# Kernel tuning notes

Measured on AMD Instinct MI355X. Metric: run time of the kernel, lower is better.

The kernel has to match this reference:

```python
import jax, jax.numpy as jnp
import numpy as np
import math

B, S, HID = 2, 4096, 768
H, D, M = 12, 64, 64  # heads, head_dim, num_landmarks
CK = 33  # conv kernel size


def setup_inputs() -> dict:
    key = jax.random.key(0)
    ks = jax.random.split(key, 4)
    x = jax.random.normal(ks[0], (B, S, HID), dtype=jnp.float32)
    qkv_w = jax.random.normal(ks[1], (3 * HID, HID), dtype=jnp.float32) * 0.02
    qkv_b = jnp.zeros((3 * HID,), dtype=jnp.float32)
    conv_w = jax.random.normal(ks[2], (H, 1, CK, 1), dtype=jnp.float32) * 0.02
    out_w = jax.random.normal(ks[3], (HID, HID), dtype=jnp.float32) * 0.02
    out_b = jnp.zeros((HID,), dtype=jnp.float32)
    return {"x": x, "qkv_w": qkv_w, "qkv_b": qkv_b, "conv_w": conv_w,
            "out_w": out_w, "out_b": out_b}


def iterative_inv(mat, n_iter=6):
    # Newton-Schulz pseudo-inverse on [B,H,M,M]
    I = jnp.eye(mat.shape[-1], dtype=mat.dtype)
    K = mat
    a = jnp.abs(K)
    scale = 1.0 / (jnp.max(jnp.sum(a, axis=-2)) * jnp.max(jnp.sum(a, axis=-1)))
    V = scale * jnp.swapaxes(K, -1, -2)
    for _ in range(n_iter):
        KV = K @ V
        V = 0.25 * V @ (13.0 * I - KV @ (15.0 * I - KV @ (7.0 * I - KV)))
    return V


def reference(x, qkv_w, qkv_b, conv_w, out_w, out_b):
    scale = 1.0 / math.sqrt(D)
    qkv = x @ qkv_w.T + qkv_b  # [B,S,3*HID]
    q, k, v = jnp.split(qkv, 3, axis=-1)
    # [B,H,S,D]
    Q = q.reshape(B, S, H, D).transpose(0, 2, 1, 3)
    K = k.reshape(B, S, H, D).transpose(0, 2, 1, 3)
    V = v.reshape(B, S, H, D).transpose(0, 2, 1, 3)
    # landmark means over contiguous segments of size S//M
    seg = S // M
    Q_l = Q.reshape(B, H, M, seg, D).mean(axis=-2)  # [B,H,M,D]
    K_l = K.reshape(B, H, M, seg, D).mean(axis=-2)
    kernel_1 = jax.nn.softmax(jnp.einsum('bhsd,bhmd->bhsm', Q, K_l) * scale, axis=-1)
    kernel_2 = jax.nn.softmax(jnp.einsum('bhmd,bhnd->bhmn', Q_l, K_l) * scale, axis=-1)
    kernel_3 = jax.nn.softmax(jnp.einsum('bhmd,bhsd->bhms', Q_l, K) * scale, axis=-1)
    X = kernel_1 @ (iterative_inv(kernel_2) @ (kernel_3 @ V))  # [B,H,S,D]
    # depthwise conv over sequence dim: NCHW with C=H, spatial=(S,D), kernel (CK,1)
    pad = CK // 2
    conv_out = jax.lax.conv_general_dilated(
        V, conv_w, window_strides=(1, 1), padding=((pad, pad), (0, 0)),
        dimension_numbers=('NCHW', 'OIHW', 'NCHW'), feature_group_count=H)
    X = X + conv_out
    X = X.transpose(0, 2, 1, 3).reshape(B, S, HID)
    X = X @ out_w.T + out_b
    return X
```

## Files before the change

kernel.cpp:

```cpp
#include <hip/hip_runtime.h>
#include <math.h>

#define B_   2
#define S_   4096
#define HID_ 768
#define H_   12
#define D_   64
#define M_   64
#define CK_  33
#define BH_  (B_*H_)
#define KD_  768
#define NCH_ 32
#define SC_  128

typedef float  f32x4  __attribute__((ext_vector_type(4)));
typedef _Float16 f16x8 __attribute__((ext_vector_type(8)));
typedef unsigned short u16;

__device__ __forceinline__ u16 f2h_bits(float f) {
  union { _Float16 h; u16 u; } c; c.h = (_Float16)f; return c.u;
}
__device__ __forceinline__ float h2f(u16 b) {
  union { _Float16 h; u16 u; } c; c.u = b; return (float)c.h;
}
__device__ __forceinline__ void cvt8_hl(const float4 a, const float4 b,
                                        f16x8* hi, f16x8* lo) {
  const float v[8] = {a.x, a.y, a.z, a.w, b.x, b.y, b.z, b.w};
  f16x8 H, L;
#pragma unroll
  for (int e = 0; e < 8; ++e) {
    const _Float16 hh = (_Float16)v[e];
    H[e] = hh;
    L[e] = (_Float16)(v[e] - (float)hh);
  }
  *hi = H; *lo = L;
}
__device__ __forceinline__ void wsplit(u16* Hh, u16* Hl, int idx, float v) {
  const _Float16 hh = (_Float16)v;
  Hh[idx] = f2h_bits(v);
  Hl[idx] = f2h_bits(v - (float)hh);
}

__device__ __forceinline__ void gld16(const void* g, void* l) {
  __builtin_amdgcn_global_load_lds(
      (const __attribute__((address_space(1))) void*)g,
      (__attribute__((address_space(3))) void*)l, 16, 0, 0);
}

#define N8X  786432
#define N8WQ 221184
#define N8WO 73728
__global__ __launch_bounds__(256) void split3(
    const float* __restrict__ x, const float* __restrict__ qkv_w,
    const float* __restrict__ out_w,
    u16* __restrict__ Xh, u16* __restrict__ Wqh, u16* __restrict__ Woh)
{
  const int i = blockIdx.x * 256 + threadIdx.x;
  const float* src; u16* dst; int j;
  if (i < N8X)                 { src = x;     dst = Xh;  j = i; }
  else if (i < N8X + N8WQ)     { src = qkv_w; dst = Wqh; j = i - N8X; }
  else if (i < N8X + N8WQ + N8WO) { src = out_w; dst = Woh; j = i - N8X - N8WQ; }
  else return;
  const float4 a = ((const float4*)src)[2 * j], b = ((const float4*)src)[2 * j + 1];
  const float v[8] = {a.x, a.y, a.z, a.w, b.x, b.y, b.z, b.w};
  union { u16 u[8]; uint4 q; } hv;
#pragma unroll
  for (int e = 0; e < 8; ++e) hv.u[e] = f2h_bits(v[e]);
  ((uint4*)dst)[j] = hv.q;
}

template<int MODE, int PROD>
__global__ __launch_bounds__(256) void gemm_mfma(
    const u16* __restrict__ Ahg, const u16* __restrict__ Alg,
    const u16* __restrict__ Bhg,
    const float* __restrict__ bias,
    float* __restrict__ oF, u16* __restrict__ oQ, u16* __restrict__ oK,
    u16* __restrict__ oV,
    float* __restrict__ Ql, float* __restrict__ Kl, u16* __restrict__ Klh)
{
  constexpr int BM = (MODE == 0) ? 128 : 64;
  constexpr int BN = (MODE == 0) ? 64 : 128;
  constexpr int NBX = (MODE == 0) ? 36 : 6;
  constexpr int WM = BM / 2, WN = BN / 2;
  constexpr int MF = WM / 16, NF = WN / 16;
  constexpr int AINST = BM / 64, BINST = BN / 64;
  constexpr int ABUF = BM * 32;
  constexpr int BUFSZ = ABUF * PROD + BN * 32;
  constexpr int NT = KD_ / 32;
  constexpr int NWG = NBX * (8192 / BM);
  constexpr int CPX = NWG / 8;
  constexpr int NLOADS = AINST * PROD + BINST;

  __shared__ __align__(16) u16 lds[2][BUFSZ];

  const int tid = threadIdx.x;
  const int lin = blockIdx.y * NBX + blockIdx.x;
  const int swb = (lin & 7) * CPX + (lin >> 3);
  const int m0 = (swb / NBX) * BM;
  const int n0 = (swb % NBX) * BN;

  const int wave = tid >> 6, lane = tid & 63;
  const int wm = wave >> 1, wn = wave & 1;
  const int lr = lane & 15, kg = lane >> 4;

  const int srow = tid >> 2;
  const int swz_s = (tid >> 3) & 3;
  const int sk = ((tid & 3) ^ swz_s) * 8;

  const u16* pAh = Ahg + (size_t)(m0 + srow) * KD_ + sk;
  const u16* pAl = (PROD == 2) ? (Alg + (size_t)(m0 + srow) * KD_ + sk) : nullptr;
  const u16* pBh = Bhg + (size_t)(n0 + srow) * KD_ + sk;

  f32x4 acc[MF][NF];
#pragma unroll
  for (int i = 0; i < MF; ++i)
#pragma unroll
    for (int j = 0; j < NF; ++j) acc[i][j] = (f32x4){0.f, 0.f, 0.f, 0.f};

  const int rsw = (lr >> 1) & 3;
  const int kq = (kg ^ rsw) * 8;
  const int abase = (wm * WM + lr) * 32 + kq;
  const int bbase = (wn * WN + lr) * 32 + kq;

#define STAGE_(buf, kt) do {                                              \
    const size_t go_ = (size_t)(kt) * 32;                                 \
    u16* L_ = &lds[buf][0];                                               \
    gld16(pAh + go_, L_ + tid * 8);                                       \
    if (AINST == 2) gld16(pAh + go_ + 64 * KD_, L_ + 2048 + tid * 8);     \
    if (PROD == 2) {                                                      \
      gld16(pAl + go_, L_ + ABUF + tid * 8);                              \
      if (AINST == 2) gld16(pAl + go_ + 64 * KD_, L_ + ABUF + 2048 + tid * 8); \
    }                                                                     \
    gld16(pBh + go_, L_ + ABUF * PROD + tid * 8);                         \
    if (BINST == 2) gld16(pBh + go_ + 64 * KD_, L_ + ABUF * PROD + 2048 + tid * 8); \
  } while (0)

  STAGE_(0, 0);

  int cur = 0;
  for (int kt = 0; kt < NT; ++kt) {
    if (kt + 1 < NT) {
      STAGE_(cur ^ 1, kt + 1);
      if constexpr (NLOADS == 3)
        asm volatile("s_waitcnt vmcnt(3)" ::: "memory");
      else
        asm volatile("s_waitcnt vmcnt(4)" ::: "memory");
    } else {
      asm volatile("s_waitcnt vmcnt(0)" ::: "memory");
    }
    __builtin_amdgcn_s_barrier();
    __builtin_amdgcn_sched_barrier(0);

    const u16* L_ = &lds[cur][0];
    f16x8 ah[MF], al[MF], bh[NF];
#pragma unroll
    for (int i = 0; i < MF; ++i) {
      ah[i] = *(const f16x8*)&L_[abase + i * 512];
      if (PROD == 2) al[i] = *(const f16x8*)&L_[ABUF + abase + i * 512];
    }
#pragma unroll
    for (int j = 0; j < NF; ++j)
      bh[j] = *(const f16x8*)&L_[ABUF * PROD + bbase + j * 512];
#pragma unroll
    for (int i = 0; i < MF; ++i)
#pragma unroll
      for (int j = 0; j < NF; ++j) {
        acc[i][j] = __builtin_amdgcn_mfma_f32_16x16x32_f16(ah[i], bh[j], acc[i][j], 0, 0, 0);
        if (PROD == 2)
          acc[i][j] = __builtin_amdgcn_mfma_f32_16x16x32_f16(al[i], bh[j], acc[i][j], 0, 0, 0);
      }

    __builtin_amdgcn_sched_barrier(0);
    __builtin_amdgcn_s_barrier();
    cur ^= 1;
  }
#undef STAGE_

  if (MODE == 0) {
    const int part = n0 / 768;
    const int h0 = (n0 - part * 768) >> 6;
    u16* base = (part == 0) ? oQ : ((part == 1) ? oK : oV);
#pragma unroll
    for (int i = 0; i < MF; ++i) {
      const int mbase = m0 + wm * WM + i * 16 + kg * 4;
#pragma unroll
      for (int j = 0; j < NF; ++j) {
        const int d = wn * WN + j * 16 + lr;
        const float bv = bias[n0 + d];
#pragma unroll
        for (int r = 0; r < 4; ++r) {
          const int row = mbase + r;
          const int b = row >> 12, s = row & (S_ - 1);
          base[(((size_t)(b * H_ + h0) * S_ + s) << 6) + d] = f2h_bits(acc[i][j][r] + bv);
        }
      }
    }
    if (part < 2) {
      const int rowseg = m0 + wm * WM;
      const int b = rowseg >> 12;
      const int seg = (rowseg & (S_ - 1)) >> 6;
      const int bhh = b * H_ + h0;
      float* dst = (part == 0) ? Ql : Kl;
#pragma unroll
      for (int j = 0; j < NF; ++j) {
        float sj = 0.f;
#pragma unroll
        for (int i = 0; i < MF; ++i)
#pragma unroll
          for (int r = 0; r < 4; ++r) sj += acc[i][j][r];
        sj += __shfl_xor(sj, 16);
        sj += __shfl_xor(sj, 32);
        if (kg == 0) {
          const int d = wn * WN + j * 16 + lr;
          const float lm = sj * (1.f / 64.f) + bias[n0 + d];
          dst[((size_t)bhh * M_ + seg) * 64 + d] = lm;
          if (part == 1) Klh[((size_t)bhh * M_ + seg) * 64 + d] = f2h_bits(lm);
        }
      }
    }
  } else {
#pragma unroll
    for (int i = 0; i < MF; ++i) {
      const int mbase = m0 + wm * WM + i * 16 + kg * 4;
#pragma unroll
      for (int j = 0; j < NF; ++j) {
        const int ncol = n0 + wn * WN + j * 16 + lr;
        const float bv = bias[ncol];
#pragma unroll
        for (int r = 0; r < 4; ++r) {
          const int row = mbase + r;
          oF[(size_t)row * HID_ + ncol] = acc[i][j][r] + bv;
        }
      }
    }
  }
}

__global__ __launch_bounds__(256) void kernel2_softmax(
    const float* __restrict__ Ql, const float* __restrict__ Kl,
    float* __restrict__ K2, float* __restrict__ colmax, float* __restrict__ rowmax)
{
  __shared__ float Qs[64][68], Ks[64][68], S2[64][68];
  __shared__ float red1[64], red2[64];
  const int bh = blockIdx.x, tid = threadIdx.x;
  for (int idx = tid; idx < 4096; idx += 256) {
    const int r = idx >> 6, c = idx & 63;
    Qs[r][c] = Ql[(size_t)bh * 4096 + idx];
    Ks[r][c] = Kl[(size_t)bh * 4096 + idx];
  }
  __syncthreads();
  for (int idx = tid; idx < 4096; idx += 256) {
    const int r = idx >> 6, c = idx & 63;
    float dot = 0.f;
#pragma unroll
    for (int k = 0; k < 64; k += 4) {
      const float4 a = *(const float4*)&Qs[r][k];
      const float4 b = *(const float4*)&Ks[c][k];
      dot += a.x * b.x + a.y * b.y + a.z * b.z + a.w * b.w;
    }
    S2[r][c] = dot * 0.125f;
  }
  __syncthreads();
  if (tid < 64) {
    const int r = tid;
    float mx = -1e30f;
    for (int c = 0; c < 64; ++c) mx = fmaxf(mx, S2[r][c]);
    float sum = 0.f;
    for (int c = 0; c < 64; ++c) { const float e = expf(S2[r][c] - mx); S2[r][c] = e; sum += e; }
    const float inv = 1.f / sum;
    for (int c = 0; c < 64; ++c) S2[r][c] *= inv;
  }
  __syncthreads();
  for (int idx = tid; idx < 4096; idx += 256)
    K2[(size_t)bh * 4096 + idx] = S2[idx >> 6][idx & 63];
  if (tid < 64) {
    float cs = 0.f, rs = 0.f;
    for (int m = 0; m < 64; ++m) { cs += S2[m][tid]; rs += S2[tid][m]; }
    red1[tid] = cs; red2[tid] = rs;
  }
  __syncthreads();
  if (tid == 0) {
    float mc = 0.f, mr = 0.f;
    for (int i = 0; i < 64; ++i) { mc = fmaxf(mc, red1[i]); mr = fmaxf(mr, red2[i]); }
    colmax[bh] = mc; rowmax[bh] = mr;
  }
}

#define NST 88
__device__ __forceinline__ void mfma64x64(
    const u16* Ah, const u16* Al, const u16* Bh, const u16* Bl,
    int wave, int lr, int kg, f32x4 C[4])
{
#pragma unroll
  for (int j = 0; j < 4; ++j) C[j] = (f32x4){0.f, 0.f, 0.f, 0.f};
#pragma unroll
  for (int kk = 0; kk < 2; ++kk) {
    const int ao = (wave * 16 + lr) * NST + kk * 32 + kg * 8;
    const f16x8 ah = *(const f16x8*)&Ah[ao];
    const f16x8 al = *(const f16x8*)&Al[ao];
#pragma unroll
    for (int j = 0; j < 4; ++j) {
      const int bo = (j * 16 + lr) * NST + kk * 32 + kg * 8;
      const f16x8 bh = *(const f16x8*)&Bh[bo];
      const f16x8 bl = *(const f16x8*)&Bl[bo];
      C[j] = __builtin_amdgcn_mfma_f32_16x16x32_f16(ah, bh, C[j], 0, 0, 0);
      C[j] = __builtin_amdgcn_mfma_f32_16x16x32_f16(ah, bl, C[j], 0, 0, 0);
      C[j] = __builtin_amdgcn_mfma_f32_16x16x32_f16(al, bh, C[j], 0, 0, 0);
    }
  }
}

__global__ __launch_bounds__(256) void newton_combine(
    const float* __restrict__ K2, const float* __restrict__ colmax,
    const float* __restrict__ rowmax,
    const float* __restrict__ Opart, const float* __restrict__ mpart,
    const float* __restrict__ lpart, float* __restrict__ W2)
{
  __shared__ __align__(16) u16 K2h[64*NST], K2l[64*NST];
  __shared__ __align__(16) u16 Vh_[64*NST], Vl_[64*NST];
  __shared__ __align__(16) u16 VTh[64*NST], VTl[64*NST];
  __shared__ __align__(16) u16 KVh[64*NST], KVl[64*NST];
  __shared__ __align__(16) u16 TTh[64*NST], TTl[64*NST];
  __shared__ float w_[64][33];
  __shared__ float scale_s;

  const int bh = blockIdx.x, tid = threadIdx.x;
  const int wave = tid >> 6, lane = tid & 63;
  const int lr = lane & 15, kg = lane >> 4;

  if (tid == 0) {
    float mc = 0.f, mr = 0.f;
    for (int i = 0; i < BH_; ++i) { mc = fmaxf(mc, colmax[i]); mr = fmaxf(mr, rowmax[i]); }
    scale_s = 1.f / (mc * mr);
  }
  __syncthreads();
  const float scale = scale_s;

  for (int idx = tid; idx < 4096; idx += 256) {
    const int r = idx >> 6, c = idx & 63;
    const float v = K2[(size_t)bh * 4096 + idx];
    wsplit(K2h, K2l, r * NST + c, v);
    const float sv = scale * v;
    wsplit(VTh, VTl, r * NST + c, sv);
    wsplit(Vh_, Vl_, c * NST + r, sv);
  }
  __syncthreads();

  f32x4 C[4];
  for (int it = 0; it < 6; ++it) {
    mfma64x64(K2h, K2l, VTh, VTl, wave, lr, kg, C);
#pragma unroll
    for (int j = 0; j < 4; ++j)
#pragma unroll
      for (int r = 0; r < 4; ++r) {
        const int row = wave * 16 + kg * 4 + r, col = j * 16 + lr;
        const float kv = C[j][r];
        wsplit(KVh, KVl, row * NST + col, kv);
        wsplit(TTh, TTl, col * NST + row, (row == col ? 7.f : 0.f) - kv);
      }
    __syncthreads();
    mfma64x64(KVh, KVl, TTh, TTl, wave, lr, kg, C);
    __syncthreads();
#pragma unroll
    for (int j = 0; j < 4; ++j)
#pragma unroll
      for (int r = 0; r < 4; ++r) {
        const int row = wave * 16 + kg * 4 + r, col = j * 16 + lr;
        wsplit(TTh, TTl, col * NST + row, (row == col ? 15.f : 0.f) - C[j][r]);
      }
    __syncthreads();
    mfma64x64(KVh, KVl, TTh, TTl, wave, lr, kg, C);
    __syncthreads();
#pragma unroll
    for (int j = 0; j < 4; ++j)
#pragma unroll
      for (int r = 0; r < 4; ++r) {
        const int row = wave * 16 + kg * 4 + r, col = j * 16 + lr;
        wsplit(TTh, TTl, col * NST + row, (row == col ? 13.f : 0.f) - C[j][r]);
      }
    __syncthreads();
    mfma64x64(Vh_, Vl_, TTh, TTl, wave, lr, kg, C);
#pragma unroll
    for (int j = 0; j < 4; ++j)
#pragma unroll
      for (int r = 0; r < 4; ++r) {
        const int row = wave * 16 + kg * 4 + r, col = j * 16 + lr;
        const float v = 0.25f * C[j][r];
        wsplit(Vh_, Vl_, row * NST + col, v);
        wsplit(VTh, VTl, col * NST + row, v);
      }
    __syncthreads();
  }

  if (tid < 64) {
    const int m = tid;
    float Mx = -1e30f;
    for (int j = 0; j < NCH_; ++j)
      Mx = fmaxf(Mx, mpart[((size_t)bh * NCH_ + j) * 64 + m]);
    float denom = 0.f;
    for (int j = 0; j < NCH_; ++j)
      denom += expf(mpart[((size_t)bh * NCH_ + j) * 64 + m] - Mx) *
               lpart[((size_t)bh * NCH_ + j) * 64 + m];
    const float inv = 1.f / denom;
    for (int j = 0; j < NCH_; ++j)
      w_[m][j] = expf(mpart[((size_t)bh * NCH_ + j) * 64 + m] - Mx) * inv;
  }
  __syncthreads();
  u16* W1Th = K2h;
  u16* W1Tl = K2l;
  {
    const int mg = tid >> 4, dq = (tid & 15) * 4;
#pragma unroll
    for (int i = 0; i < 4; ++i) {
      const int m = mg * 4 + i;
      float4 acc = make_float4(0.f, 0.f, 0.f, 0.f);
      for (int j = 0; j < NCH_; ++j) {
        const float ww = w_[m][j];
        const float4 o = *(const float4*)&Opart[(((size_t)bh * NCH_ + j) * 64 + m) * 64 + dq];
        acc.x += ww * o.x; acc.y += ww * o.y; acc.z += ww * o.z; acc.w += ww * o.w;
      }
      wsplit(W1Th, W1Tl, (dq + 0) * NST + m, acc.x);
      wsplit(W1Th, W1Tl, (dq + 1) * NST + m, acc.y);
      wsplit(W1Th, W1Tl, (dq + 2) * NST + m, acc.z);
      wsplit(W1Th, W1Tl, (dq + 3) * NST + m, acc.w);
    }
  }
  __syncthreads();
  mfma64x64(Vh_, Vl_, W1Th, W1Tl, wave, lr, kg, C);
#pragma unroll
  for (int j = 0; j < 4; ++j)
#pragma unroll
    for (int r = 0; r < 4; ++r) {
      const int row = wave * 16 + kg * 4 + r, col = j * 16 + lr;
      W2[(size_t)bh * 4096 + row * 64 + col] = C[j][r];
    }
}

__global__ __launch_bounds__(256) void k3v_pass1(
    const float* __restrict__ Ql, const u16* __restrict__ Kh,
    const u16* __restrict__ Vh, float* __restrict__ Opart,
    float* __restrict__ mpart, float* __restrict__ lpart)
{
  __shared__ float P[64][129];
  __shared__ float red1[64][4], red2[64][4];

  const int ch = blockIdx.x;
  const int bh = blockIdx.y;
  const int tid = threadIdx.x;
  const int wave = tid >> 6, lane = tid & 63;
  const int lr = lane & 15, kg = lane >> 4;

  const float* Qlb = Ql + (size_t)bh * 4096;
  const u16*   Kb  = Kh + (size_t)bh * S_ * 64;
  const u16*   Vb  = Vh + (size_t)bh * S_ * 64;

  f16x8 ah[4][2], al[4][2];
#pragma unroll
  for (int mt = 0; mt < 4; ++mt)
#pragma unroll
    for (int kk = 0; kk < 2; ++kk) {
      const float* qr = Qlb + (size_t)(mt * 16 + lr) * 64 + kk * 32 + kg * 8;
      cvt8_hl(*(const float4*)qr, *(const float4*)(qr + 4), &ah[mt][kk], &al[mt][kk]);
    }

#pragma unroll
  for (int t = 0; t < 2; ++t) {
    const int s0 = (wave * 2 + t) * 16;
    const int srow = ch * SC_ + s0 + lr;
    f32x4 acc[4];
#pragma unroll
    for (int mt = 0; mt < 4; ++mt) acc[mt] = (f32x4){0.f, 0.f, 0.f, 0.f};
#pragma unroll
    for (int kk = 0; kk < 2; ++kk) {
      const f16x8 bhf = *(const f16x8*)&Kb[(size_t)srow * 64 + kk * 32 + kg * 8];
#pragma unroll
      for (int mt = 0; mt < 4; ++mt) {
        acc[mt] = __builtin_amdgcn_mfma_f32_16x16x32_f16(ah[mt][kk], bhf, acc[mt], 0, 0, 0);
        acc[mt] = __builtin_amdgcn_mfma_f32_16x16x32_f16(al[mt][kk], bhf, acc[mt], 0, 0, 0);
      }
    }
#pragma unroll
    for (int mt = 0; mt < 4; ++mt)
#pragma unroll
      for (int r = 0; r < 4; ++r)
        P[mt * 16 + kg * 4 + r][s0 + lr] = acc[mt][r] * 0.125f;
  }
  __syncthreads();

  const int r = tid >> 2, q = tid & 3;
  {
    float mx = -1e30f;
#pragma unroll
    for (int s = 0; s < 32; ++s) mx = fmaxf(mx, P[r][q * 32 + s]);
    red1[r][q] = mx;
  }
  __syncthreads();
  const float rowmax = fmaxf(fmaxf(red1[r][0], red1[r][1]),
                             fmaxf(red1[r][2], red1[r][3]));
  {
    float sum = 0.f;
#pragma unroll
    for (int s = 0; s < 32; ++s) {
      const float e = expf(P[r][q * 32 + s] - rowmax);
      P[r][q * 32 + s] = e;
      sum += e;
    }
    red2[r][q] = sum;
  }
  __syncthreads();
  if (q == 0) {
    const float rowsum = red2[r][0] + red2[r][1] + red2[r][2] + red2[r][3];
    mpart[((size_t)bh * NCH_ + ch) * 64 + r] = rowmax;
    lpart[((size_t)bh * NCH_ + ch) * 64 + r] = rowsum;
  }

  const int mg = tid >> 4, dq = (tid & 15) * 4;
  float4 oacc[4];
#pragma unroll
  for (int i = 0; i < 4; ++i) oacc[i] = make_float4(0.f, 0.f, 0.f, 0.f);
  for (int s = 0; s < SC_; ++s) {
    const ushort4 vv = *(const ushort4*)&Vb[(size_t)(ch * SC_ + s) * 64 + dq];
    const float4 v = make_float4(h2f(vv.x), h2f(vv.y), h2f(vv.z), h2f(vv.w));
#pragma unroll
    for (int i = 0; i < 4; ++i) {
      const float p = P[mg * 4 + i][s];
      oacc[i].x += p * v.x; oacc[i].y += p * v.y;
      oacc[i].z += p * v.z; oacc[i].w += p * v.w;
    }
  }
#pragma unroll
  for (int i = 0; i < 4; ++i) {
    const size_t o = (((size_t)bh * NCH_ + ch) * 64 + mg * 4 + i) * 64 + dq;
    *(float4*)&Opart[o] = oacc[i];
  }
}

__global__ __launch_bounds__(256) void attn_conv_fused(
    const u16* __restrict__ Qh, const u16* __restrict__ Klh,
    const float* __restrict__ W2, const u16* __restrict__ Vh,
    const float* __restrict__ cw,
    u16* __restrict__ Xch, u16* __restrict__ Xcl)
{
  __shared__ __align__(16) u16 smem[19456];
  __shared__ float cws[33];

  const int ch = blockIdx.x;
  const int bh = blockIdx.y;
  const int tid = threadIdx.x;
  const int wave = tid >> 6, lane = tid & 63;
  const int lr = lane & 15, kg = lane >> 4;
  const int b = bh / H_, h = bh % H_;
  const int s0 = ch * 128;

  u16* Ph   = smem;
  u16* W2Th = smem + 9728;
  u16* W2Tl = smem + 14592;

  if (tid < 33) cws[tid] = cw[h * 33 + tid];
  for (int idx = tid; idx < 4096; idx += 256) {
    const int m = idx >> 6, d = idx & 63;
    const float w = W2[(size_t)bh * 4096 + idx];
    const _Float16 hh = (_Float16)w;
    W2Th[d * 76 + m] = f2h_bits(w);
    W2Tl[d * 76 + m] = f2h_bits(w - (float)hh);
  }

  const u16* Klb = Klh + (size_t)bh * 4096;
  const u16* Qb  = Qh + (size_t)bh * S_ * 64;
  f16x8 bf[4][2];
#pragma unroll
  for (int nt = 0; nt < 4; ++nt)
#pragma unroll
    for (int kk = 0; kk < 2; ++kk)
      bf[nt][kk] = *(const f16x8*)&Klb[(size_t)(nt * 16 + lr) * 64 + kk * 32 + kg * 8];

  f32x4 sacc[2][4];
#pragma unroll
  for (int t = 0; t < 2; ++t) {
#pragma unroll
    for (int nt = 0; nt < 4; ++nt) sacc[t][nt] = (f32x4){0.f, 0.f, 0.f, 0.f};
    const int rloc = wave * 32 + t * 16;
    f16x8 af[2];
#pragma unroll
    for (int kk = 0; kk < 2; ++kk)
      af[kk] = *(const f16x8*)&Qb[(size_t)(s0 + rloc + lr) * 64 + kk * 32 + kg * 8];
#pragma unroll
    for (int kk = 0; kk < 2; ++kk)
#pragma unroll
      for (int nt = 0; nt < 4; ++nt)
        sacc[t][nt] = __builtin_amdgcn_mfma_f32_16x16x32_f16(af[kk], bf[nt][kk], sacc[t][nt], 0, 0, 0);
  }

#pragma unroll
  for (int t = 0; t < 2; ++t)
#pragma unroll
    for (int nt = 0; nt < 4; ++nt)
      sacc[t][nt] *= 0.125f;

  float rinv[2][4];
#pragma unroll
  for (int t = 0; t < 2; ++t) {
#pragma unroll
    for (int r = 0; r < 4; ++r) {
      float mx = fmaxf(fmaxf(sacc[t][0][r], sacc[t][1][r]),
                       fmaxf(sacc[t][2][r], sacc[t][3][r]));
      mx = fmaxf(mx, __shfl_xor(mx, 1));
      mx = fmaxf(mx, __shfl_xor(mx, 2));
      mx = fmaxf(mx, __shfl_xor(mx, 4));
      mx = fmaxf(mx, __shfl_xor(mx, 8));
      float sum = 0.f;
#pragma unroll
      for (int nt = 0; nt < 4; ++nt) {
        const float e = expf(sacc[t][nt][r] - mx);
        sacc[t][nt][r] = e;
        sum += e;
      }
      sum += __shfl_xor(sum, 1);
      sum += __shfl_xor(sum, 2);
      sum += __shfl_xor(sum, 4);
      sum += __shfl_xor(sum, 8);
      rinv[t][r] = 1.f / sum;
    }
  }

#pragma unroll
  for (int t = 0; t < 2; ++t)
#pragma unroll
    for (int nt = 0; nt < 4; ++nt)
#pragma unroll
      for (int r = 0; r < 4; ++r) {
        const int row = wave * 32 + t * 16 + kg * 4 + r;
        Ph[row * 76 + nt * 16 + lr] = f2h_bits(sacc[t][nt][r] * rinv[t][r]);
      }
  __syncthreads();

  f32x4 oacc[2][4];
#pragma unroll
  for (int t = 0; t < 2; ++t)
#pragma unroll
    for (int dt = 0; dt < 4; ++dt) oacc[t][dt] = (f32x4){0.f, 0.f, 0.f, 0.f};
#pragma unroll
  for (int kk = 0; kk < 2; ++kk) {
    f16x8 pa[2];
#pragma unroll
    for (int t = 0; t < 2; ++t)
      pa[t] = *(const f16x8*)&Ph[(wave * 32 + t * 16 + lr) * 76 + kk * 32 + kg * 8];
#pragma unroll
    for (int dt = 0; dt < 4; ++dt) {
      const f16x8 wh = *(const f16x8*)&W2Th[(dt * 16 + lr) * 76 + kk * 32 + kg * 8];
      const f16x8 wl = *(const f16x8*)&W2Tl[(dt * 16 + lr) * 76 + kk * 32 + kg * 8];
#pragma unroll
      for (int t = 0; t < 2; ++t) {
        oacc[t][dt] = __builtin_amdgcn_mfma_f32_16x16x32_f16(pa[t], wh, oacc[t][dt], 0, 0, 0);
        oacc[t][dt] = __builtin_amdgcn_mfma_f32_16x16x32_f16(pa[t], wl, oacc[t][dt], 0, 0, 0);
      }
    }
  }
  __syncthreads();

  float* O = (float*)smem;
#pragma unroll
  for (int t = 0; t < 2; ++t)
#pragma unroll
    for (int dt = 0; dt < 4; ++dt)
#pragma unroll
      for (int r = 0; r < 4; ++r) {
        const int row = wave * 32 + t * 16 + kg * 4 + r;
        O[row * 68 + dt * 16 + lr] = oacc[t][dt][r];
      }
  __syncthreads();

  const int d = tid & 63, rg = tid >> 6;
  const int rbase = s0 + rg * 32;
  const u16* Vd = Vh + (size_t)bh * S_ * 64 + d;

  float v[40];
#pragma unroll
  for (int j = 0; j < 40; ++j) {
    const int sv = rbase - 16 + j;
    v[j] = (sv >= 0 && sv < S_) ? h2f(Vd[(size_t)sv * 64]) : 0.f;
  }

#pragma clang loop unroll(disable)
  for (int c = 0; c < 4; ++c) {
#pragma unroll
    for (int rr = 0; rr < 8; ++rr) {
      float acc = 0.f;
#pragma unroll
      for (int t = 0; t < 33; ++t) acc += v[rr + t] * cws[t];
      const int row = rg * 32 + c * 8 + rr;
      const float oo = O[row * 68 + d] + acc;
      const size_t idx = ((size_t)(b * S_ + s0 + row)) * HID_ + h * 64 + d;
      const u16 hh = f2h_bits(oo);
      Xch[idx] = hh;
      Xcl[idx] = f2h_bits(oo - h2f(hh));
    }
    if (c < 3) {
#pragma unroll
      for (int j = 0; j < 32; ++j) v[j] = v[j + 8];
#pragma unroll
      for (int j = 0; j < 8; ++j) {
        const int sv = rbase + 24 + c * 8 + j;
        v[32 + j] = (sv >= 0 && sv < S_) ? h2f(Vd[(size_t)sv * 64]) : 0.f;
      }
    }
  }
}

extern "C" void kernel_launch(void* const* d_in, const int* in_sizes, int n_in,
                              void* d_out, int out_size, void* d_ws, size_t ws_size,
                              hipStream_t stream)
{
  (void)in_sizes; (void)n_in; (void)out_size; (void)ws_size;
  const float* x      = (const float*)d_in[0];
  const float* qkv_w  = (const float*)d_in[1];
  const float* qkv_b  = (const float*)d_in[2];
  const float* conv_w = (const float*)d_in[3];
  const float* out_w  = (const float*)d_in[4];
  const float* out_b  = (const float*)d_in[5];
  float* out = (float*)d_out;

  float* ws = (float*)d_ws;
  u16* Qh = (u16*)ws;
  u16* Kh = Qh + 6291456;
  u16* Vh = Kh + 6291456;
  float* Ql = ws + 9437184;
  float* Kl = Ql + 98304;
  float* K2 = Kl + 98304;
  float* W2 = K2 + 98304;
  float* colmax = W2 + 98304;
  float* rowmax = colmax + 32;
  u16* Klh = (u16*)(rowmax + 32);
  float* nxt = rowmax + 32 + 49152;
  u16* Xh  = (u16*)nxt;
  u16* Xl  = Xh + 6291456;
  u16* Wqh = Xl + 6291456;
  u16* Woh = Wqh + 1769472;
  u16* Xch = Xh;
  u16* Xcl = Xl;
  float* Opart = (float*)Xh;
  float* mpart = (float*)Xl;
  float* lpart = mpart + BH_ * NCH_ * 64;

  split3<<<(N8X + N8WQ + N8WO + 255) / 256, 256, 0, stream>>>(
      x, qkv_w, out_w, Xh, Wqh, Woh);

  gemm_mfma<0, 1><<<dim3(36, 64), 256, 0, stream>>>(
      Xh, nullptr, Wqh, qkv_b, nullptr, Qh, Kh, Vh, Ql, Kl, Klh);

  kernel2_softmax<<<BH_, 256, 0, stream>>>(Ql, Kl, K2, colmax, rowmax);

  k3v_pass1<<<dim3(NCH_, BH_), 256, 0, stream>>>(Ql, Kh, Vh, Opart, mpart, lpart);

  newton_combine<<<BH_, 256, 0, stream>>>(K2, colmax, rowmax,
                                          Opart, mpart, lpart, W2);

  attn_conv_fused<<<dim3(NCH_, BH_), 256, 0, stream>>>(
      Qh, Klh, W2, Vh, conv_w, Xch, Xcl);

  gemm_mfma<1, 2><<<dim3(6, 128), 256, 0, stream>>>(
      Xch, Xcl, Woh, out_b, out, nullptr, nullptr, nullptr,
      nullptr, nullptr, nullptr);
}
```

Before: 212.3 us.

## Use per-wave private LDS tiles in GEMMs and drop fp16 split-precision output

```diff
diff --git a/kernel.cpp b/kernel.cpp
--- a/kernel.cpp
+++ b/kernel.cpp
@@ -69,124 +69,102 @@
   ((uint4*)dst)[j] = hv.q;
 }
 
-template<int MODE, int PROD>
-__global__ __launch_bounds__(256) void gemm_mfma(
-    const u16* __restrict__ Ahg, const u16* __restrict__ Alg,
-    const u16* __restrict__ Bhg,
+template<int MODE>
+__global__ __launch_bounds__(256) void gemm_wave(
+    const u16* __restrict__ Ahg, const u16* __restrict__ Bhg,
     const float* __restrict__ bias,
     float* __restrict__ oF, u16* __restrict__ oQ, u16* __restrict__ oK,
     u16* __restrict__ oV,
     float* __restrict__ Ql, float* __restrict__ Kl, u16* __restrict__ Klh)
 {
-  constexpr int BM = (MODE == 0) ? 128 : 64;
-  constexpr int BN = (MODE == 0) ? 64 : 128;
-  constexpr int NBX = (MODE == 0) ? 36 : 6;
-  constexpr int WM = BM / 2, WN = BN / 2;
-  constexpr int MF = WM / 16, NF = WN / 16;
-  constexpr int AINST = BM / 64, BINST = BN / 64;
-  constexpr int ABUF = BM * 32;
-  constexpr int BUFSZ = ABUF * PROD + BN * 32;
-  constexpr int NT = KD_ / 32;
-  constexpr int NWG = NBX * (8192 / BM);
+  constexpr int NBX = (MODE == 0) ? 18 : 6;
+  constexpr int NT  = KD_ / 32;
+  constexpr int NWG = NBX * 64;
   constexpr int CPX = NWG / 8;
-  constexpr int NLOADS = AINST * PROD + BINST;
-
-  __shared__ __align__(16) u16 lds[2][BUFSZ];
+
+  __shared__ __align__(16) u16 lds[4][2][2][2048];
 
   const int tid = threadIdx.x;
   const int lin = blockIdx.y * NBX + blockIdx.x;
   const int swb = (lin & 7) * CPX + (lin >> 3);
-  const int m0 = (swb / NBX) * BM;
-  const int n0 = (swb % NBX) * BN;
+  const int m0 = (swb / NBX) * 128;
+  const int n0 = (swb % NBX) * 128;
 
   const int wave = tid >> 6, lane = tid & 63;
   const int wm = wave >> 1, wn = wave & 1;
   const int lr = lane & 15, kg = lane >> 4;
 
-  const int srow = tid >> 2;
-  const int swz_s = (tid >> 3) & 3;
-  const int sk = ((tid & 3) ^ swz_s) * 8;
-
-  const u16* pAh = Ahg + (size_t)(m0 + srow) * KD_ + sk;
-  const u16* pAl = (PROD == 2) ? (Alg + (size_t)(m0 + srow) * KD_ + sk) : nullptr;
-  const u16* pBh = Bhg + (size_t)(n0 + srow) * KD_ + sk;
-
-  f32x4 acc[MF][NF];
-#pragma unroll
-  for (int i = 0; i < MF; ++i)
-#pragma unroll
-    for (int j = 0; j < NF; ++j) acc[i][j] = (f32x4){0.f, 0.f, 0.f, 0.f};
-
-  const int rsw = (lr >> 1) & 3;
-  const int kq = (kg ^ rsw) * 8;
-  const int abase = (wm * WM + lr) * 32 + kq;
-  const int bbase = (wn * WN + lr) * 32 + kq;
-
-#define STAGE_(buf, kt) do {                                              \
-    const size_t go_ = (size_t)(kt) * 32;                                 \
-    u16* L_ = &lds[buf][0];                                               \
-    gld16(pAh + go_, L_ + tid * 8);                                       \
-    if (AINST == 2) gld16(pAh + go_ + 64 * KD_, L_ + 2048 + tid * 8);     \
-    if (PROD == 2) {                                                      \
-      gld16(pAl + go_, L_ + ABUF + tid * 8);                              \
-      if (AINST == 2) gld16(pAl + go_ + 64 * KD_, L_ + ABUF + 2048 + tid * 8); \
-    }                                                                     \
-    gld16(pBh + go_, L_ + ABUF * PROD + tid * 8);                         \
-    if (BINST == 2) gld16(pBh + go_ + 64 * KD_, L_ + ABUF * PROD + 2048 + tid * 8); \
+  const int srow = lane >> 2;
+  const int sk = ((lane & 3) ^ ((lane >> 3) & 3)) * 8;
+
+  const u16* pA = Ahg + (size_t)(m0 + wm * 64 + srow) * KD_ + sk;
+  const u16* pB = Bhg + (size_t)(n0 + wn * 64 + srow) * KD_ + sk;
+
+  u16* wbase = &lds[wave][0][0][0];
+
+  f32x4 acc[4][4];
+#pragma unroll
+  for (int i = 0; i < 4; ++i)
+#pragma unroll
+    for (int j = 0; j < 4; ++j) acc[i][j] = (f32x4){0.f, 0.f, 0.f, 0.f};
+
+  const int kq = (kg ^ ((lr >> 1) & 3)) * 8;
+
+#define WSTAGE_(buf, kt) do {                                   \
+    const size_t go_ = (size_t)(kt) * 32;                       \
+    u16* La_ = wbase + (buf) * 4096 + lane * 8;                 \
+    u16* Lb_ = La_ + 2048;                                      \
+    gld16(pA + go_,              La_);                          \
+    gld16(pA + go_ + 16 * KD_,   La_ + 512);                    \
+    gld16(pA + go_ + 32 * KD_,   La_ + 1024);                   \
+    gld16(pA + go_ + 48 * KD_,   La_ + 1536);                   \
+    gld16(pB + go_,              Lb_);                          \
+    gld16(pB + go_ + 16 * KD_,   Lb_ + 512);                    \
+    gld16(pB + go_ + 32 * KD_,   Lb_ + 1024);                   \
+    gld16(pB + go_ + 48 * KD_,   Lb_ + 1536);                   \
   } while (0)
 
-  STAGE_(0, 0);
+  WSTAGE_(0, 0);
 
   int cur = 0;
   for (int kt = 0; kt < NT; ++kt) {
     if (kt + 1 < NT) {
-      STAGE_(cur ^ 1, kt + 1);
-      if constexpr (NLOADS == 3)
-        asm volatile("s_waitcnt vmcnt(3)" ::: "memory");
-      else
-        asm volatile("s_waitcnt vmcnt(4)" ::: "memory");
+      WSTAGE_(cur ^ 1, kt + 1);
+      asm volatile("s_waitcnt vmcnt(8)" ::: "memory");
     } else {
       asm volatile("s_waitcnt vmcnt(0)" ::: "memory");
     }
-    __builtin_amdgcn_s_barrier();
     __builtin_amdgcn_sched_barrier(0);
 
-    const u16* L_ = &lds[cur][0];
-    f16x8 ah[MF], al[MF], bh[NF];
-#pragma unroll
-    for (int i = 0; i < MF; ++i) {
-      ah[i] = *(const f16x8*)&L_[abase + i * 512];
-      if (PROD == 2) al[i] = *(const f16x8*)&L_[ABUF + abase + i * 512];
-    }
-#pragma unroll
-    for (int j = 0; j < NF; ++j)
-      bh[j] = *(const f16x8*)&L_[ABUF * PROD + bbase + j * 512];
-#pragma unroll
-    for (int i = 0; i < MF; ++i)
-#pragma unroll
-      for (int j = 0; j < NF; ++j) {
-        acc[i][j] = __builtin_amdgcn_mfma_f32_16x16x32_f16(ah[i], bh[j], acc[i][j], 0, 0, 0);
-        if (PROD == 2)
-          acc[i][j] = __builtin_amdgcn_mfma_f32_16x16x32_f16(al[i], bh[j], acc[i][j], 0, 0, 0);
-      }
-
-    __builtin_amdgcn_sched_barrier(0);
-    __builtin_amdgcn_s_barrier();
+    const u16* Abuf = wbase + cur * 4096;
+    const u16* Bbuf = Abuf + 2048;
+    f16x8 af[4], bf[4];
+#pragma unroll
+    for (int i = 0; i < 4; ++i) af[i] = *(const f16x8*)&Abuf[(i * 16 + lr) * 32 + kq];
+#pragma unroll
+    for (int j = 0; j < 4; ++j) bf[j] = *(const f16x8*)&Bbuf[(j * 16 + lr) * 32 + kq];
+#pragma unroll
+    for (int i = 0; i < 4; ++i)
+#pragma unroll
+      for (int j = 0; j < 4; ++j)
+        acc[i][j] = __builtin_amdgcn_mfma_f32_16x16x32_f16(af[i], bf[j], acc[i][j], 0, 0, 0);
+
     cur ^= 1;
   }
-#undef STAGE_
+#undef WSTAGE_
 
   if (MODE == 0) {
     const int part = n0 / 768;
-    const int h0 = (n0 - part * 768) >> 6;
+    const int within0 = n0 + wn * 64 - part * 768;
+    const int h0 = within0 >> 6;
     u16* base = (part == 0) ? oQ : ((part == 1) ? oK : oV);
 #pragma unroll
-    for (int i = 0; i < MF; ++i) {
-      const int mbase = m0 + wm * WM + i * 16 + kg * 4;
-#pragma unroll
-      for (int j = 0; j < NF; ++j) {
-        const int d = wn * WN + j * 16 + lr;
-        const float bv = bias[n0 + d];
+    for (int i = 0; i < 4; ++i) {
+      const int mbase = m0 + wm * 64 + i * 16 + kg * 4;
+#pragma unroll
+      for (int j = 0; j < 4; ++j) {
+        const int d = j * 16 + lr;
+        const float bv = bias[n0 + wn * 64 + d];
 #pragma unroll
         for (int r = 0; r < 4; ++r) {
           const int row = mbase + r;
@@ -196,23 +174,23 @@
       }
     }
     if (part < 2) {
-      const int rowseg = m0 + wm * WM;
+      const int rowseg = m0 + wm * 64;
       const int b = rowseg >> 12;
       const int seg = (rowseg & (S_ - 1)) >> 6;
       const int bhh = b * H_ + h0;
       float* dst = (part == 0) ? Ql : Kl;
 #pragma unroll
-      for (int j = 0; j < NF; ++j) {
+      for (int j = 0; j < 4; ++j) {
         float sj = 0.f;
 #pragma unroll
-        for (int i = 0; i < MF; ++i)
+        for (int i = 0; i < 4; ++i)
 #pragma unroll
           for (int r = 0; r < 4; ++r) sj += acc[i][j][r];
         sj += __shfl_xor(sj, 16);
         sj += __shfl_xor(sj, 32);
         if (kg == 0) {
-          const int d = wn * WN + j * 16 + lr;
-          const float lm = sj * (1.f / 64.f) + bias[n0 + d];
+          const int d = j * 16 + lr;
+          const float lm = sj * (1.f / 64.f) + bias[n0 + wn * 64 + d];
           dst[((size_t)bhh * M_ + seg) * 64 + d] = lm;
           if (part == 1) Klh[((size_t)bhh * M_ + seg) * 64 + d] = f2h_bits(lm);
         }
@@ -220,11 +198,11 @@
     }
   } else {
 #pragma unroll
-    for (int i = 0; i < MF; ++i) {
-      const int mbase = m0 + wm * WM + i * 16 + kg * 4;
-#pragma unroll
-      for (int j = 0; j < NF; ++j) {
-        const int ncol = n0 + wn * WN + j * 16 + lr;
+    for (int i = 0; i < 4; ++i) {
+      const int mbase = m0 + wm * 64 + i * 16 + kg * 4;
+#pragma unroll
+      for (int j = 0; j < 4; ++j) {
+        const int ncol = n0 + wn * 64 + j * 16 + lr;
         const float bv = bias[ncol];
 #pragma unroll
         for (int r = 0; r < 4; ++r) {
@@ -538,8 +516,7 @@
 __global__ __launch_bounds__(256) void attn_conv_fused(
     const u16* __restrict__ Qh, const u16* __restrict__ Klh,
     const float* __restrict__ W2, const u16* __restrict__ Vh,
-    const float* __restrict__ cw,
-    u16* __restrict__ Xch, u16* __restrict__ Xcl)
+    const float* __restrict__ cw, u16* __restrict__ Xch)
 {
   __shared__ __align__(16) u16 smem[19456];
   __shared__ float cws[33];
@@ -691,9 +668,7 @@
       const int row = rg * 32 + c * 8 + rr;
       const float oo = O[row * 68 + d] + acc;
       const size_t idx = ((size_t)(b * S_ + s0 + row)) * HID_ + h * 64 + d;
-      const u16 hh = f2h_bits(oo);
-      Xch[idx] = hh;
-      Xcl[idx] = f2h_bits(oo - h2f(hh));
+      Xch[idx] = f2h_bits(oo);
     }
     if (c < 3) {
 #pragma unroll
@@ -737,7 +712,6 @@
   u16* Wqh = Xl + 6291456;
   u16* Woh = Wqh + 1769472;
   u16* Xch = Xh;
-  u16* Xcl = Xl;
   float* Opart = (float*)Xh;
   float* mpart = (float*)Xl;
   float* lpart = mpart + BH_ * NCH_ * 64;
@@ -745,8 +719,8 @@
   split3<<<(N8X + N8WQ + N8WO + 255) / 256, 256, 0, stream>>>(
       x, qkv_w, out_w, Xh, Wqh, Woh);
 
-  gemm_mfma<0, 1><<<dim3(36, 64), 256, 0, stream>>>(
-      Xh, nullptr, Wqh, qkv_b, nullptr, Qh, Kh, Vh, Ql, Kl, Klh);
+  gemm_wave<0><<<dim3(18, 64), 256, 0, stream>>>(
+      Xh, Wqh, qkv_b, nullptr, Qh, Kh, Vh, Ql, Kl, Klh);
 
   kernel2_softmax<<<BH_, 256, 0, stream>>>(Ql, Kl, K2, colmax, rowmax);
 
@@ -756,9 +730,9 @@
                                           Opart, mpart, lpart, W2);
 
   attn_conv_fused<<<dim3(NCH_, BH_), 256, 0, stream>>>(
-      Qh, Klh, W2, Vh, conv_w, Xch, Xcl);
-
-  gemm_mfma<1, 2><<<dim3(6, 128), 256, 0, stream>>>(
-      Xch, Xcl, Woh, out_b, out, nullptr, nullptr, nullptr,
+      Qh, Klh, W2, Vh, conv_w, Xch);
+
+  gemm_wave<1><<<dim3(6, 64), 256, 0, stream>>>(
+      Xch, Woh, out_b, out, nullptr, nullptr, nullptr,
       nullptr, nullptr, nullptr);
 }
```

Result: no change. 211.7 us (-0.3%).
